# Optimization experiments

Measured on AMD Instinct MI355X. Metric: run time of the kernel, lower is better.

The kernel has to match this reference:

```python
import jax, jax.numpy as jnp
import numpy as np

B, G, D = 16, 20000, 64   # batch, num_genes, feature_dim
S, L = 500, 128           # num_gene_sets, max genes per set (padded)


def setup_inputs() -> dict:
    key = jax.random.key(0)
    k1, k2, k3 = jax.random.split(key, 3)
    gene_features = jax.random.normal(k1, (B, G, D), dtype=jnp.float32)
    geneset_indices = jax.random.randint(k2, (S, L), 0, G, dtype=jnp.int32)
    set_mask = jnp.ones((S, L), dtype=bool)  # all positions valid (uniform-size sets)
    attn_weights = jax.random.normal(k3, (S, L, D), dtype=jnp.float32)
    return {
        "gene_features": gene_features,
        "attn_weights": attn_weights,
        "geneset_indices": geneset_indices,
        "set_mask": set_mask,
    }


def reference(gene_features, attn_weights, geneset_indices, set_mask):
    # Gather per-set gene features: [B, S, L, D]
    gathered = jnp.take(gene_features, geneset_indices, axis=1)
    # Masked softmax over the set-member axis L (independent per feature dim),
    # matching F.softmax(attention_weights, dim=1) per gene set.
    neg = jnp.finfo(attn_weights.dtype).min
    logits = jnp.where(set_mask[:, :, None], attn_weights, neg)  # [S, L, D]
    attn = jax.nn.softmax(logits, axis=1)                        # [S, L, D]
    # Weighted sum over set members -> [B, S, D]
    return jnp.einsum('bsld,sld->bsd', gathered, attn)
```

## Files before the change

### kernel.cpp

```cpp
#include <hip/hip_runtime.h>
#include <math.h>


#define NB 16
#define NG 20000
#define ND 64
#define NS 500
#define NL 128

typedef unsigned short ushortx8 __attribute__((ext_vector_type(8)));
typedef float floatx8 __attribute__((ext_vector_type(8)));

__device__ __forceinline__ float bf2f(unsigned short u) {
    union { unsigned int i; float f; } x;
    x.i = ((unsigned int)u) << 16;
    return x.f;
}

__device__ __forceinline__ unsigned short f2bf(float f) {
    union { float f; unsigned int i; } x;
    x.f = f;
    unsigned int r = x.i + 0x7FFFu + ((x.i >> 16) & 1u);
    return (unsigned short)(r >> 16);
}

__device__ __forceinline__ void lgkm_barrier() {
    asm volatile("s_waitcnt lgkmcnt(0)" ::: "memory");
    __builtin_amdgcn_s_barrier();
}

__global__ void detect_dtype_kernel(const unsigned short* __restrict__ aw,
                                    int* __restrict__ flag) {
    const unsigned int e = ((unsigned int)aw[2 * threadIdx.x] >> 7) & 0xFFu;
    const unsigned long long m = __ballot(e >= 100u && e <= 135u);
    if (threadIdx.x == 0) *flag = (__popcll(m) >= 32) ? 1 : 0;
}

template<bool BF16>
__global__ __launch_bounds__(1024)
void agg_kernel(const void* __restrict__ gf_,
                const void* __restrict__ aw_,
                const int*  __restrict__ idx,
                void*       __restrict__ out_,
                const int*  __restrict__ flag)
{
    if (*flag != (BF16 ? 1 : 0)) return;

    __shared__ float attn_s[NL * ND];
    __shared__ float red[16 * ND];
    __shared__ int   gidx[NL];

    const int s = blockIdx.x;
    const int t = threadIdx.x;

    if (t < NL) gidx[t] = idx[s * NL + t];

    const int d    = t & 63;
    const int part = t >> 6;
    const unsigned short* awp = (const unsigned short*)aw_ + (size_t)s * (NL * ND);

    float m = -INFINITY;
    #pragma unroll
    for (int i = 0; i < 8; ++i) {
        const int l = part * 8 + i;
        const float v = BF16 ? bf2f(awp[l * ND + d])
                             : ((const float*)aw_)[(size_t)s * (NL * ND) + l * ND + d];
        attn_s[l * ND + d] = v;
        m = fmaxf(m, v);
    }
    red[part * ND + d] = m;
    lgkm_barrier();

    float m_all = -INFINITY;
    #pragma unroll
    for (int p = 0; p < 16; ++p) m_all = fmaxf(m_all, red[p * ND + d]);

    const int b    = t >> 6;
    const int lane = t & 63;
    const int lp   = lane >> 3;
    const int q    = lane & 7;
    const int d0   = q * 8;

    float acc[8];
    #pragma unroll
    for (int j = 0; j < 8; ++j) acc[j] = 0.f;

    if (BF16) {
        const unsigned short* gb = (const unsigned short*)gf_ + (size_t)b * (NG * ND) + d0;
        int4 ub[16];

        asm volatile("s_waitcnt vmcnt(0)" ::: "memory");

#define ISSUE(k) do {                                                         \
            const int g_ = gidx[lp * 16 + (k)];                               \
            const unsigned long long a_ =                                     \
                (unsigned long long)(gb + (size_t)g_ * ND);                   \
            asm volatile("global_load_dwordx4 %0, %1, off"                    \
                         : "=v"(ub[(k)]) : "v"(a_));                          \
        } while (0)
        ISSUE(0);  ISSUE(1);  ISSUE(2);  ISSUE(3);
        ISSUE(4);  ISSUE(5);  ISSUE(6);  ISSUE(7);
        ISSUE(8);  ISSUE(9);  ISSUE(10); ISSUE(11);
        ISSUE(12); ISSUE(13); ISSUE(14); ISSUE(15);
#undef ISSUE

        lgkm_barrier();

        float psum = 0.f;
        #pragma unroll
        for (int i = 0; i < 8; ++i) {
            const int l = part * 8 + i;
            const float e = __expf(attn_s[l * ND + d] - m_all);
            attn_s[l * ND + d] = e;
            psum += e;
        }
        red[part * ND + d] = psum;
        lgkm_barrier();

#define CONSUME(k, cnt) do {                                                  \
            asm volatile("s_waitcnt vmcnt(" #cnt ")");                        \
            __builtin_amdgcn_sched_barrier(0);                                \
            const floatx8 w_ =                                                \
                *(const floatx8*)&attn_s[(lp * 16 + (k)) * ND + d0];          \
            const ushortx8 u_ = *(const ushortx8*)&ub[(k)];                   \
            _Pragma("unroll")                                                 \
            for (int j = 0; j < 8; ++j) acc[j] += bf2f(u_[j]) * w_[j];        \
        } while (0)
        CONSUME(0, 15);  CONSUME(1, 14);  CONSUME(2, 13);  CONSUME(3, 12);
        CONSUME(4, 11);  CONSUME(5, 10);  CONSUME(6, 9);   CONSUME(7, 8);
        CONSUME(8, 7);   CONSUME(9, 6);   CONSUME(10, 5);  CONSUME(11, 4);
        CONSUME(12, 3);  CONSUME(13, 2);  CONSUME(14, 1);  CONSUME(15, 0);
#undef CONSUME
    } else {
        lgkm_barrier();

        float psum = 0.f;
        #pragma unroll
        for (int i = 0; i < 8; ++i) {
            const int l = part * 8 + i;
            const float e = __expf(attn_s[l * ND + d] - m_all);
            attn_s[l * ND + d] = e;
            psum += e;
        }
        red[part * ND + d] = psum;
        lgkm_barrier();

        const float* gb = (const float*)gf_ + (size_t)b * (NG * ND) + d0;
        floatx8 uf[4];
        #pragma unroll
        for (int k = 0; k < 4; ++k) {
            const int g = gidx[lp * 16 + k];
            uf[k] = *(const floatx8*)(gb + (size_t)g * ND);
        }
        #pragma unroll
        for (int k = 0; k < 16; ++k) {
            const int l = lp * 16 + k;
            const floatx8 w = *(const floatx8*)&attn_s[l * ND + d0];
            const floatx8 uk = uf[k & 3];
            if (k + 4 < 16) {
                const int g = gidx[lp * 16 + k + 4];
                uf[k & 3] = *(const floatx8*)(gb + (size_t)g * ND);
            }
            #pragma unroll
            for (int j = 0; j < 8; ++j) acc[j] += uk[j] * w[j];
        }
    }

    #pragma unroll
    for (int j = 0; j < 8; ++j) {
        acc[j] += __shfl_xor(acc[j], 8);
        acc[j] += __shfl_xor(acc[j], 16);
        acc[j] += __shfl_xor(acc[j], 32);
    }

    if (lp == 0) {
        floatx8 tot;
        #pragma unroll
        for (int j = 0; j < 8; ++j) tot[j] = 0.f;
        #pragma unroll
        for (int p = 0; p < 16; ++p) tot += *(const floatx8*)&red[p * ND + d0];
        if (BF16) {
            ushortx8 o;
            #pragma unroll
            for (int j = 0; j < 8; ++j) o[j] = f2bf(acc[j] * (1.0f / tot[j]));
            *(ushortx8*)((unsigned short*)out_ + ((size_t)b * NS + s) * ND + d0) = o;
        } else {
            floatx8 o;
            #pragma unroll
            for (int j = 0; j < 8; ++j) o[j] = acc[j] * (1.0f / tot[j]);
            *(floatx8*)((float*)out_ + ((size_t)b * NS + s) * ND + d0) = o;
        }
    }
}

extern "C" void kernel_launch(void* const* d_in, const int* in_sizes, int n_in,
                              void* d_out, int out_size, void* d_ws, size_t ws_size,
                              hipStream_t stream) {
    const void* gf  = d_in[0];
    const void* aw  = d_in[1];
    const int*  idx = (const int*)d_in[2];
    int* flag = (int*)d_ws;

    detect_dtype_kernel<<<1, 64, 0, stream>>>((const unsigned short*)aw, flag);
    agg_kernel<true ><<<NS, 1024, 0, stream>>>(gf, aw, idx, d_out, flag);
    agg_kernel<false><<<NS, 1024, 0, stream>>>(gf, aw, idx, d_out, flag);
}
```

Before: 155.7 us.

## Stage bf16 gene gathers through LDS with a 4-deep ring buffer

Replaces 16 in-flight register-destination global loads per lane with direct global-to-LDS loads (global_load_lds) into a 4-slot per-wave staging ring, refilling each slot after it is consumed. The aim is to cut VGPR pressure from the 16 int4 buffers and keep a steady rolling prefetch. The cost is 64KB of extra shared memory per block and lower memory-level parallelism (4 loads in flight instead of 16), plus extra LDS reads and lgkmcnt waits per step.

```diff
diff --git a/kernel.cpp b/kernel.cpp
--- a/kernel.cpp
+++ b/kernel.cpp
@@ -49,6 +49,7 @@
     __shared__ float attn_s[NL * ND];
     __shared__ float red[16 * ND];
     __shared__ int   gidx[NL];
+    __shared__ __align__(16) char stage[16 * 4 * 1024];
 
     const int s = blockIdx.x;
     const int t = threadIdx.x;
@@ -86,23 +87,22 @@
     for (int j = 0; j < 8; ++j) acc[j] = 0.f;
 
     if (BF16) {
-        const unsigned short* gb = (const unsigned short*)gf_ + (size_t)b * (NG * ND) + d0;
-        int4 ub[16];
+        const unsigned short* gb_lane =
+            (const unsigned short*)gf_ + (size_t)b * (NG * ND) + d0;
+        char* stage_w = &stage[b * 4096];
+
+#define GL_ISSUE(k) do {                                                      \
+            const int g_ = gidx[lp * 16 + (k)];                               \
+            const unsigned short* s_ = gb_lane + (size_t)g_ * ND;             \
+            __builtin_amdgcn_global_load_lds(                                 \
+                (const __attribute__((address_space(1))) unsigned int*)s_,    \
+                (__attribute__((address_space(3))) unsigned int*)              \
+                    (stage_w + ((k) & 3) * 1024),                             \
+                16, 0, 0);                                                    \
+        } while (0)
 
         asm volatile("s_waitcnt vmcnt(0)" ::: "memory");
-
-#define ISSUE(k) do {                                                         \
-            const int g_ = gidx[lp * 16 + (k)];                               \
-            const unsigned long long a_ =                                     \
-                (unsigned long long)(gb + (size_t)g_ * ND);                   \
-            asm volatile("global_load_dwordx4 %0, %1, off"                    \
-                         : "=v"(ub[(k)]) : "v"(a_));                          \
-        } while (0)
-        ISSUE(0);  ISSUE(1);  ISSUE(2);  ISSUE(3);
-        ISSUE(4);  ISSUE(5);  ISSUE(6);  ISSUE(7);
-        ISSUE(8);  ISSUE(9);  ISSUE(10); ISSUE(11);
-        ISSUE(12); ISSUE(13); ISSUE(14); ISSUE(15);
-#undef ISSUE
+        GL_ISSUE(0); GL_ISSUE(1); GL_ISSUE(2); GL_ISSUE(3);
 
         lgkm_barrier();
 
@@ -118,19 +118,25 @@
         lgkm_barrier();
 
 #define CONSUME(k, cnt) do {                                                  \
-            asm volatile("s_waitcnt vmcnt(" #cnt ")");                        \
+            asm volatile("s_waitcnt vmcnt(" #cnt ")" ::: "memory");           \
             __builtin_amdgcn_sched_barrier(0);                                \
-            const floatx8 w_ =                                                \
+            const ushortx8 u_ = *(const ushortx8*)(stage_w +                  \
+                                    ((k) & 3) * 1024 + lane * 16);            \
+            const floatx8  w_ =                                               \
                 *(const floatx8*)&attn_s[(lp * 16 + (k)) * ND + d0];          \
-            const ushortx8 u_ = *(const ushortx8*)&ub[(k)];                   \
+            asm volatile("s_waitcnt lgkmcnt(0)" ::: "memory");                \
+            __builtin_amdgcn_sched_barrier(0);                                \
+            if ((k) + 4 < 16) GL_ISSUE((k) + 4);                              \
             _Pragma("unroll")                                                 \
             for (int j = 0; j < 8; ++j) acc[j] += bf2f(u_[j]) * w_[j];        \
         } while (0)
-        CONSUME(0, 15);  CONSUME(1, 14);  CONSUME(2, 13);  CONSUME(3, 12);
-        CONSUME(4, 11);  CONSUME(5, 10);  CONSUME(6, 9);   CONSUME(7, 8);
-        CONSUME(8, 7);   CONSUME(9, 6);   CONSUME(10, 5);  CONSUME(11, 4);
+
+        CONSUME(0, 3);   CONSUME(1, 3);   CONSUME(2, 3);   CONSUME(3, 3);
+        CONSUME(4, 3);   CONSUME(5, 3);   CONSUME(6, 3);   CONSUME(7, 3);
+        CONSUME(8, 3);   CONSUME(9, 3);   CONSUME(10, 3);  CONSUME(11, 3);
         CONSUME(12, 3);  CONSUME(13, 2);  CONSUME(14, 1);  CONSUME(15, 0);
 #undef CONSUME
+#undef GL_ISSUE
     } else {
         lgkm_barrier();
 
```

After: 156.3 us. About the same (+0.4%).
